# Kernel optimization log

Measured on AMD Instinct MI355X. Metric: run time of the kernel, lower is better.

Reference implementation:

```python
import jax, jax.numpy as jnp
import numpy as np

NUM_CODES = 4096
EMBED_DIM = 64
BETA = 0.25


def setup_inputs() -> dict:
    key = jax.random.key(0)
    k1, k2 = jax.random.split(key)
    z = jax.random.normal(k1, (8, EMBED_DIM, 64, 64), dtype=jnp.float32)
    weight = jax.random.normal(k2, (NUM_CODES, EMBED_DIM), dtype=jnp.float32)
    return {"z": z, "weight": weight}


def reference(z, weight):
    # z: [B, C, H, W] -> [B, H, W, C]
    z_bhwc = jnp.moveaxis(z, 1, -1)
    z_flat = z_bhwc.reshape(-1, EMBED_DIM)  # [N, d]

    # squared-euclidean distances: ||z||^2 + ||w||^2 - 2 z.w  -> [N, num_codes]
    distance = (
        jnp.sum(z_flat ** 2, axis=1, keepdims=True)
        + jnp.sum(weight ** 2, axis=1)
        - 2.0 * jnp.einsum('bd,nd->bn', z_flat, weight)
    )
    encoding_indices = jnp.argmin(distance, axis=1)  # [N]

    # codebook lookup (gather)
    z_q = weight[encoding_indices].reshape(z_bhwc.shape)  # [B, H, W, C]

    encodings = jax.nn.one_hot(encoding_indices, NUM_CODES, dtype=z.dtype)  # [N, num_codes]
    avg_probs = jnp.mean(encodings, axis=0)
    tiny = 1e-10  # max(1e-10, finfo(fp32).tiny)
    perplexity = jnp.exp(-jnp.sum(avg_probs * jnp.log(avg_probs + tiny)))

    # commitment loss (z_q detached) — eval path, no EMA state update
    loss = BETA * jnp.mean((jax.lax.stop_gradient(z_q) - z_bhwc) ** 2)

    # straight-through estimator
    z_q = z_bhwc + jax.lax.stop_gradient(z_q - z_bhwc)
    z_q = jnp.moveaxis(z_q, -1, 1)  # back to [B, C, H, W]

    return z_q, loss, perplexity, encodings, encoding_indices
```

## Files before the change

### kernel.cpp

```cpp
#include <hip/hip_runtime.h>
#include <math.h>
#include <float.h>

#define ZQ_OFF   0
#define LOSS_OFF 2097152
#define PERP_OFF 2097153
#define ENC_OFF  2097154
#define IDX_OFF  136314882ULL
#define BETA     0.25f


typedef __attribute__((ext_vector_type(8))) short short8;
typedef __attribute__((ext_vector_type(4))) float f32x4;

#define MFMA16(a, b, c) __builtin_amdgcn_mfma_f32_16x16x32_bf16(a, b, c, 0, 0, 0)

__device__ __forceinline__ float bf16_rn(float v, unsigned short* h) {
    unsigned u = __float_as_uint(v);
    unsigned r = (u + 0x7fffu + ((u >> 16) & 1u)) & 0xffff0000u;
    *h = (unsigned short)(r >> 16);
    return __uint_as_float(r);
}
__device__ __forceinline__ void split3(float v, unsigned short* h, unsigned short* m, unsigned short* l) {
    float hf = bf16_rn(v, h);
    float r1 = v - hf;
    float mf = bf16_rn(r1, m);
    float r2 = r1 - mf;
    bf16_rn(r2, l);
}

__global__ void vq_wnorm(const float* __restrict__ w, float* __restrict__ wnorm) {
    int c = blockIdx.x * 256 + threadIdx.x;
    const float4* w4 = (const float4*)(w + ((size_t)c << 6));
    float s = 0.f;
    #pragma unroll
    for (int k = 0; k < 16; ++k) { float4 v = w4[k]; s += v.x*v.x + v.y*v.y + v.z*v.z + v.w*v.w; }
    wnorm[c] = s;
}

__global__ void vq_prep(const float* __restrict__ w, unsigned short* __restrict__ w3) {
    int u = blockIdx.x * 256 + threadIdx.x;
    int c = u >> 5, slot = u & 31;
    if (slot >= 24) return;
    int p = slot >> 3, g = slot & 7;
    float4 v0 = *(const float4*)(w + ((size_t)c << 6) + g * 8);
    float4 v1 = *(const float4*)(w + ((size_t)c << 6) + g * 8 + 4);
    float vv[8] = {v0.x, v0.y, v0.z, v0.w, v1.x, v1.y, v1.z, v1.w};
    short8 o;
    #pragma unroll
    for (int e = 0; e < 8; ++e) {
        unsigned short h, m, l;
        split3(vv[e], &h, &m, &l);
        o[e] = (short)((p == 0) ? h : (p == 1) ? m : l);
    }
    char* dst = (char*)w3 + (size_t)c * 384 + (((unsigned)slot * 16) ^ (((unsigned)c & 7) << 4));
    *(short8*)dst = o;
}

__global__ __launch_bounds__(256, 4) void vq_main(
    const float* __restrict__ z, const float* __restrict__ w,
    const float* __restrict__ wnorm, const unsigned short* __restrict__ w3,
    float* __restrict__ out,
    float* __restrict__ loss_ws, int* __restrict__ ticket, int* __restrict__ hist)
{
    __shared__ __align__(16) char wl[24576];
    __shared__ int s_widx[64];
    __shared__ int s_flag;

    const int tx   = threadIdx.x;
    const int lane = tx & 63;
    const int wv   = tx >> 6;
    const int lcol = lane & 15;
    const int lkq  = lane >> 4;
    const int base = blockIdx.x * 64;
    const int bb   = base >> 12;
    const int hh   = (base & 4095) >> 6;

    float (*zS)[64] = (float (*)[64])wl;
    #pragma unroll
    for (int j = 0; j < 4; ++j) {
        int f4 = j * 256 + tx;
        int d  = f4 >> 4, w4i = f4 & 15;
        float4 v = *(const float4*)(z + (((size_t)bb * 64 + d) * 64 + hh) * 64 + w4i * 4);
        *(float4*)&zS[d][w4i * 4] = v;
    }
    __syncthreads();

    short8 aH[2], aM[2], aL[2];
    #pragma unroll
    for (int s = 0; s < 2; ++s)
        #pragma unroll
        for (int j = 0; j < 8; ++j) {
            float v = zS[s * 32 + lkq * 8 + j][wv * 16 + lcol];
            unsigned short h, m, l;
            split3(v, &h, &m, &l);
            aH[s][j] = (short)h; aM[s][j] = (short)m; aL[s][j] = (short)l;
        }
    __syncthreads();

    float best[4]; int bidx[4];
    #pragma unroll
    for (int r = 0; r < 4; ++r) { best[r] = FLT_MAX; bidx[r] = 0; }

    float* enc = out + ENC_OFF;
    const char* w3b  = (const char*)w3;
    const char* wsrc = w3b + wv * 6144 + lane * 16;
    char*       wdst = wl  + wv * 6144;

    const unsigned sw = ((unsigned)lcol & 7) << 4;

    #pragma unroll 1
    for (int ch = 0; ch < 64; ++ch) {
        {
            const char* s0 = wsrc + (size_t)ch * 24576;
            #pragma unroll
            for (int i = 0; i < 6; ++i)
                __builtin_amdgcn_global_load_lds(
                    (const __attribute__((address_space(1))) void*)(s0 + i * 1024),
                    (__attribute__((address_space(3))) void*)(wdst + i * 1024), 16, 0, 0);
        }
        {
            float2* rowp = (float2*)(enc + ((size_t)(base + ch) << 12));
            #pragma unroll
            for (int j = 0; j < 8; ++j)
                rowp[wv * 512 + j * 64 + lane] = make_float2(0.f, 0.f);
        }
        __syncthreads();

        {
            const int cbase = ch << 6;
            float wnv[4];
            #pragma unroll
            for (int t = 0; t < 4; ++t) wnv[t] = wnorm[cbase + t * 16 + lcol];
            #pragma unroll 2
            for (int t = 0; t < 4; ++t) {
                const int clocal = t * 16 + lcol;
                const char* rowp = wl + clocal * 384;
                short8 bH0 = *(const short8*)(rowp + ((lkq * 16      ) ^ sw));
                short8 bH1 = *(const short8*)(rowp + ((lkq * 16 +  64) ^ sw));
                short8 bM0 = *(const short8*)(rowp + ((lkq * 16 + 128) ^ sw));
                short8 bM1 = *(const short8*)(rowp + ((lkq * 16 + 192) ^ sw));
                short8 bL0 = *(const short8*)(rowp + ((lkq * 16 + 256) ^ sw));
                short8 bL1 = *(const short8*)(rowp + ((lkq * 16 + 320) ^ sw));
                f32x4 c0 = {0.f, 0.f, 0.f, 0.f}, c1 = {0.f, 0.f, 0.f, 0.f}, c2 = {0.f, 0.f, 0.f, 0.f};
                c0 = MFMA16(aH[0], bH0, c0); c0 = MFMA16(aH[1], bH1, c0);
                c1 = MFMA16(aH[0], bM0, c1); c1 = MFMA16(aH[1], bM1, c1);
                c1 = MFMA16(aM[0], bH0, c1); c1 = MFMA16(aM[1], bH1, c1);
                c2 = MFMA16(aM[0], bM0, c2); c2 = MFMA16(aM[1], bM1, c2);
                c2 = MFMA16(aH[0], bL0, c2); c2 = MFMA16(aH[1], bL1, c2);
                c2 = MFMA16(aL[0], bH0, c2); c2 = MFMA16(aL[1], bH1, c2);
                #pragma unroll
                for (int r = 0; r < 4; ++r) {
                    float sdot = (c0[r] + c1[r]) + c2[r];
                    float dd = fmaf(-2.f, sdot, wnv[t]);
                    if (dd < best[r]) { best[r] = dd; bidx[r] = cbase + clocal; }
                }
            }
        }
        __syncthreads();
    }

    #pragma unroll
    for (int mm = 1; mm < 16; mm <<= 1) {
        #pragma unroll
        for (int r = 0; r < 4; ++r) {
            float ob = __shfl_xor(best[r], mm, 64);
            int   oi = __shfl_xor(bidx[r], mm, 64);
            if (ob < best[r] || (ob == best[r] && oi < bidx[r])) { best[r] = ob; bidx[r] = oi; }
        }
    }

    if (lcol == 0) {
        const int rowb = wv * 16 + lkq * 4;
        #pragma unroll
        for (int r = 0; r < 4; ++r) {
            int row = rowb + r, bi = bidx[r];
            s_widx[row] = bi;
            out[IDX_OFF + (size_t)(base + row)] = (float)bi;
            atomicAdd(&hist[bi], 1);
            enc[((size_t)(base + row) << 12) + bi] = 1.0f;
        }
    }
    __syncthreads();

    {
        const int row = tx & 63;
        const int dg  = tx >> 6;
        const int wi  = s_widx[row];
        const float* qrow = w + ((size_t)wi << 6);
        float lsum = 0.f;
        #pragma unroll
        for (int dd = 0; dd < 16; ++dd) {
            int d = dg * 16 + dd;
            float qv = qrow[d];
            float zv = z[(((size_t)bb * 64 + d) * 64 + hh) * 64 + row];
            float diff = qv - zv;
            lsum += diff * diff;
            out[ZQ_OFF + (((size_t)bb * 64 + d) * 64 + hh) * 64 + row] = zv + (qv - zv);
        }
        #pragma unroll
        for (int off = 32; off > 0; off >>= 1) lsum += __shfl_down(lsum, off, 64);
        if ((tx & 63) == 0) atomicAdd(loss_ws, lsum);
    }

    __syncthreads();
    if (tx == 0) {
        __threadfence();
        int old = atomicAdd(ticket, 1);
        s_flag = (old == 511) ? 1 : 0;
    }
    __syncthreads();
    if (s_flag) {
        __threadfence();
        float s = 0.f;
        #pragma unroll
        for (int j = 0; j < 16; ++j) {
            int c = tx + j * 256;
            int cnt = atomicAdd(&hist[c], 0);
            float p = (float)cnt * (1.f / 32768.f);
            s += p * logf(p + 1e-10f);
        }
        float* fr = (float*)wl;
        fr[tx] = s;
        __syncthreads();
        for (int off = 128; off > 0; off >>= 1) {
            if (tx < off) fr[tx] += fr[tx + off];
            __syncthreads();
        }
        if (tx == 0) {
            out[LOSS_OFF] = BETA * atomicAdd(loss_ws, 0.f) / 2097152.f;
            out[PERP_OFF] = expf(-fr[0]);
        }
    }
}

extern "C" void kernel_launch(void* const* d_in, const int* in_sizes, int n_in,
                              void* d_out, int out_size, void* d_ws, size_t ws_size,
                              hipStream_t stream)
{
    const float* z = (const float*)d_in[0];
    const float* w = (const float*)d_in[1];
    float* out     = (float*)d_out;
    float* loss_ws = (float*)d_ws;
    int*   ticket  = (int*)((char*)d_ws + 4);
    int*   hist    = (int*)((char*)d_ws + 16);
    float* wnorm   = (float*)((char*)d_ws + 16400);
    unsigned short* w3 = (unsigned short*)((char*)d_ws + 32800);
    (void)ws_size; (void)in_sizes; (void)n_in; (void)out_size;

    hipMemsetAsync(d_ws, 0, 16 + 4096 * sizeof(int), stream);
    vq_wnorm<<<16, 256, 0, stream>>>(w, wnorm);
    vq_prep<<<512, 256, 0, stream>>>(w, w3);
    vq_main<<<512, 256, 0, stream>>>(z, w, wnorm, w3, out, loss_ws, ticket, hist);
}
```

Baseline: 653.6 us.

## Double-buffer codebook chunks in LDS and cache code norms in shared memory

```diff
diff --git a/kernel.cpp b/kernel.cpp
--- a/kernel.cpp
+++ b/kernel.cpp
@@ -57,13 +57,14 @@
     *(short8*)dst = o;
 }
 
-__global__ __launch_bounds__(256, 4) void vq_main(
+__global__ __launch_bounds__(256, 2) void vq_main(
     const float* __restrict__ z, const float* __restrict__ w,
     const float* __restrict__ wnorm, const unsigned short* __restrict__ w3,
     float* __restrict__ out,
     float* __restrict__ loss_ws, int* __restrict__ ticket, int* __restrict__ hist)
 {
-    __shared__ __align__(16) char wl[24576];
+    __shared__ __align__(16) char wl[2 * 24576];
+    __shared__ float snorm[4096];
     __shared__ int s_widx[64];
     __shared__ int s_flag;
 
@@ -76,7 +77,19 @@
     const int bb   = base >> 12;
     const int hh   = (base & 4095) >> 6;
 
-    float (*zS)[64] = (float (*)[64])wl;
+    const char* w3b = (const char*)w3;
+
+    {
+        const char* s0 = w3b + wv * 6144 + (size_t)lane * 16;
+        char* d0 = wl + wv * 6144;
+        #pragma unroll
+        for (int i = 0; i < 6; ++i)
+            __builtin_amdgcn_global_load_lds(
+                (const __attribute__((address_space(1))) void*)(s0 + i * 1024),
+                (__attribute__((address_space(3))) void*)(d0 + i * 1024), 16, 0, 0);
+    }
+
+    float (*zS)[64] = (float (*)[64])(wl + 24576);
     #pragma unroll
     for (int j = 0; j < 4; ++j) {
         int f4 = j * 256 + tx;
@@ -84,6 +97,11 @@
         float4 v = *(const float4*)(z + (((size_t)bb * 64 + d) * 64 + hh) * 64 + w4i * 4);
         *(float4*)&zS[d][w4i * 4] = v;
     }
+    #pragma unroll
+    for (int j = 0; j < 4; ++j) {
+        int c4 = (j * 256 + tx) * 4;
+        *(float4*)&snorm[c4] = *(const float4*)(wnorm + c4);
+    }
     __syncthreads();
 
     short8 aH[2], aM[2], aL[2];
@@ -96,28 +114,30 @@
             split3(v, &h, &m, &l);
             aH[s][j] = (short)h; aM[s][j] = (short)m; aL[s][j] = (short)l;
         }
-    __syncthreads();
+    __builtin_amdgcn_sched_barrier(0);
+    __builtin_amdgcn_s_barrier();
+    __builtin_amdgcn_sched_barrier(0);
 
     float best[4]; int bidx[4];
     #pragma unroll
     for (int r = 0; r < 4; ++r) { best[r] = FLT_MAX; bidx[r] = 0; }
 
     float* enc = out + ENC_OFF;
-    const char* w3b  = (const char*)w3;
-    const char* wsrc = w3b + wv * 6144 + lane * 16;
-    char*       wdst = wl  + wv * 6144;
-
     const unsigned sw = ((unsigned)lcol & 7) << 4;
 
     #pragma unroll 1
     for (int ch = 0; ch < 64; ++ch) {
+        const char* cur = wl + (ch & 1) * 24576;
+        char*       nxt = wl + (~ch & 1) * 24576;
+
         {
-            const char* s0 = wsrc + (size_t)ch * 24576;
+            const char* s0 = w3b + (size_t)((ch + 1) & 63) * 24576 + wv * 6144 + (size_t)lane * 16;
+            char* d0 = nxt + wv * 6144;
             #pragma unroll
             for (int i = 0; i < 6; ++i)
                 __builtin_amdgcn_global_load_lds(
                     (const __attribute__((address_space(1))) void*)(s0 + i * 1024),
-                    (__attribute__((address_space(3))) void*)(wdst + i * 1024), 16, 0, 0);
+                    (__attribute__((address_space(3))) void*)(d0 + i * 1024), 16, 0, 0);
         }
         {
             float2* rowp = (float2*)(enc + ((size_t)(base + ch) << 12));
@@ -125,17 +145,20 @@
             for (int j = 0; j < 8; ++j)
                 rowp[wv * 512 + j * 64 + lane] = make_float2(0.f, 0.f);
         }
-        __syncthreads();
+        __builtin_amdgcn_sched_barrier(0);
+        asm volatile("s_waitcnt vmcnt(14)" ::: "memory");
+        __builtin_amdgcn_s_barrier();
+        __builtin_amdgcn_sched_barrier(0);
 
         {
             const int cbase = ch << 6;
             float wnv[4];
             #pragma unroll
-            for (int t = 0; t < 4; ++t) wnv[t] = wnorm[cbase + t * 16 + lcol];
+            for (int t = 0; t < 4; ++t) wnv[t] = snorm[cbase + t * 16 + lcol];
             #pragma unroll 2
             for (int t = 0; t < 4; ++t) {
                 const int clocal = t * 16 + lcol;
-                const char* rowp = wl + clocal * 384;
+                const char* rowp = cur + clocal * 384;
                 short8 bH0 = *(const short8*)(rowp + ((lkq * 16      ) ^ sw));
                 short8 bH1 = *(const short8*)(rowp + ((lkq * 16 +  64) ^ sw));
                 short8 bM0 = *(const short8*)(rowp + ((lkq * 16 + 128) ^ sw));
@@ -157,8 +180,11 @@
                 }
             }
         }
-        __syncthreads();
-    }
+        __builtin_amdgcn_sched_barrier(0);
+        __builtin_amdgcn_s_barrier();
+    }
+
+    __syncthreads();
 
     #pragma unroll
     for (int mm = 1; mm < 16; mm <<= 1) {
@@ -220,7 +246,7 @@
             float p = (float)cnt * (1.f / 32768.f);
             s += p * logf(p + 1e-10f);
         }
-        float* fr = (float*)wl;
+        float* fr = snorm;
         fr[tx] = s;
         __syncthreads();
         for (int off = 128; off > 0; off >>= 1) {
```

New measurement: 612.9 us. 6.2% less time.
